# Optimization experiments

Hardware: AMD Instinct MI355X
Metric: run time of the kernel (lower is better)

## Reference

```python
import jax, jax.numpy as jnp
import numpy as np

NUM_HEADS = 4
HEAD_DIM = 64
IN_CH = 192
KERNEL_SIZES = (3, 5, 7, 9)  # per-head neighborhood size
NEG_INF = -1e30


def setup_inputs() -> dict:
    key = jax.random.key(0)
    k1, k2, k3 = jax.random.split(key, 3)
    x = jax.random.normal(k1, (8, IN_CH, 96, 96), dtype=jnp.float32)
    # QKV conv: out_channels = head_dim * num_heads * 3 = 768, 3x3, pad 1
    w_qkv = jax.random.normal(k2, (HEAD_DIM * NUM_HEADS * 3, IN_CH, 3, 3), dtype=jnp.float32) * 0.02
    b_qkv = jax.random.normal(k3, (HEAD_DIM * NUM_HEADS * 3,), dtype=jnp.float32) * 0.02
    return {"x": x, "w_qkv": w_qkv, "b_qkv": b_qkv}


def _neighborhood_attention(q, k, v, ksize):
    # q, k, v: [N, H, W, D]; KxK zero-padded neighborhood attention with
    # out-of-bounds positions masked out.
    N, H, W, D = q.shape
    pad = ksize // 2
    kp = jnp.pad(k, ((0, 0), (pad, pad), (pad, pad), (0, 0)))
    vp = jnp.pad(v, ((0, 0), (pad, pad), (pad, pad), (0, 0)))
    scale = 1.0 / np.sqrt(D).astype(np.float32)
    rows = jnp.arange(H)
    cols = jnp.arange(W)
    scores, masks = [], []
    for di in range(ksize):
        for dj in range(ksize):
            k_sh = kp[:, di:di + H, dj:dj + W, :]           # shifted keys
            scores.append(jnp.einsum('nhwd,nhwd->nhw', q, k_sh))
            rv = (rows + di - pad >= 0) & (rows + di - pad < H)   # [H]
            cv = (cols + dj - pad >= 0) & (cols + dj - pad < W)   # [W]
            masks.append(rv[:, None] & cv[None, :])               # [H, W]
    scores = jnp.stack(scores, axis=-1) * scale                   # [N,H,W,K2]
    mask = jnp.stack(masks, axis=-1)[None]                        # [1,H,W,K2]
    scores = jnp.where(mask, scores, NEG_INF)
    attn = jax.nn.softmax(scores, axis=-1)                        # [N,H,W,K2]
    out = jnp.zeros_like(q)
    t = 0
    for di in range(ksize):
        for dj in range(ksize):
            out = out + attn[..., t, None] * vp[:, di:di + H, dj:dj + W, :]
            t += 1
    return out  # [N,H,W,D]


def reference(x, w_qkv, b_qkv):
    # Dense QKV projection (Conv2d, stride 1, padding 1 == SAME for k=3)
    qkv = jax.lax.conv_general_dilated(
        x, w_qkv, window_strides=(1, 1), padding='SAME',
        dimension_numbers=('NCHW', 'OIHW', 'NCHW'))
    qkv = qkv + b_qkv[None, :, None, None]
    # transform_to_nhw1c: NCHW -> NHWC, then split channels into
    # num_heads blocks of 3*head_dim, each split into q, k, v.
    N, C, H, W = qkv.shape
    qkv = jnp.transpose(qkv, (0, 2, 3, 1)).reshape(N, H, W, NUM_HEADS, 3, HEAD_DIM)
    outs = []
    for h, ks in enumerate(KERNEL_SIZES):
        q = qkv[..., h, 0, :]
        k = qkv[..., h, 1, :]
        v = qkv[..., h, 2, :]
        o = _neighborhood_attention(q, k, v, ks)       # [N,H,W,D]
        outs.append(jnp.transpose(o, (0, 3, 1, 2)))    # transform_from_nhw1c -> NCHW
    return jnp.stack(outs, axis=0)  # [num_heads, N, D, H, W]
```

## Files before the change

kernel.cpp:

```cpp
#include <hip/hip_runtime.h>
#include <hip/hip_bf16.h>

#define NH 96
#define NW 96
#define NB 8
#define CIN 192
#define COUT 768
#define PH 98

typedef __attribute__((ext_vector_type(8))) unsigned short ushort8;
typedef __attribute__((ext_vector_type(8))) short bf16x8;
typedef __attribute__((ext_vector_type(4))) float f32x4;

static __device__ __forceinline__ unsigned short f2bf(float f) {
    unsigned int u = __float_as_uint(f);
    return (unsigned short)((u + 0x7fffu + ((u >> 16) & 1u)) >> 16);
}

typedef const __attribute__((address_space(1))) unsigned int gu32;
typedef __attribute__((address_space(3))) unsigned int lu32;
static __device__ __forceinline__ void gload16(const void* g, void* l) {
    __builtin_amdgcn_global_load_lds((gu32*)g, (lu32*)l, 16, 0, 0);
}

__global__ __launch_bounds__(256) void pack_x_kernel(
    const float* __restrict__ x, unsigned short* __restrict__ xp)
{
    __shared__ float tile[32][97];
    int bid = blockIdx.x;
    int ct = bid % 6; int y = (bid / 6) % NH; int n = bid / (6 * NH);
    int tid = threadIdx.x;
    int c0 = ct * 32;
    for (int i = tid; i < 32 * 96; i += 256) {
        int c = i / 96, xx = i % 96;
        tile[c][xx] = x[(((size_t)n * CIN + c0 + c) * NH + y) * NW + xx];
    }
    __syncthreads();
    for (int i = tid; i < 96 * 4; i += 256) {
        int xx = i >> 2, ch = i & 3;
        ushort8 pk;
#pragma unroll
        for (int j = 0; j < 8; ++j) pk[j] = f2bf(tile[ch * 8 + j][xx]);
        *(ushort8*)(xp + ((size_t)(n * PH + y + 1) * PH + xx + 1) * CIN + c0 + ch * 8) = pk;
    }
}

__global__ __launch_bounds__(256) void pack_w_kernel(
    const float* __restrict__ w, unsigned short* __restrict__ bw)
{
    __shared__ float ls[1728];
    int co = blockIdx.x; int tid = threadIdx.x;
    for (int i = tid; i < 1728; i += 256) ls[i] = w[(size_t)co * 1728 + i];
    __syncthreads();
    for (int i = tid; i < 1728; i += 256) {
        int sh = i / 192, ci = i % 192;
        bw[(size_t)co * 1728 + i] = f2bf(ls[ci * 9 + sh]);
    }
}

__global__ __launch_bounds__(512) void conv_gemm_kernel(
    const unsigned short* __restrict__ xp, const unsigned short* __restrict__ bw,
    const float* __restrict__ bias, unsigned short* __restrict__ qkq,
    unsigned short* __restrict__ vt)
{
    __shared__ __align__(16) char smem[131072];
    int bid = (blockIdx.x & 7) * 108 + (blockIdx.x >> 3);
    int brow = (bid / 3) * 256, bcol = (bid % 3) * 256;
    int tid = threadIdx.x, lane = tid & 63;
    int wid = tid >> 6, wm = wid >> 2, wn = wid & 3;
    int g = lane >> 4;

    const unsigned short* srcA[2][2];
    const unsigned short* srcB[2][2];
#pragma unroll
    for (int h = 0; h < 2; ++h)
#pragma unroll
        for (int i = 0; i < 2; ++i) {
            int s = i * 512 + tid;
            int rl = s >> 3, c = s & 7;
            int csw = (c ^ (rl & 7)) << 3;
            int p = brow + h * 128 + rl;
            int n = p / 9216; int rem = p - n * 9216;
            int y = rem / 96; int xx = rem - y * 96;
            srcA[h][i] = xp + ((size_t)(n * PH + y) * PH + xx) * CIN + csw;
            srcB[h][i] = bw + (size_t)(bcol + h * 128 + rl) * 1728 + csw;
        }
    int dsto[2];
#pragma unroll
    for (int i = 0; i < 2; ++i) dsto[i] = (i * 512 + (tid & ~63)) * 16;

#define STAGEU(T, U, BUF)                                                      \
    {                                                                          \
        int shift_ = (T) / 3, kk_ = (T) % 3;                                   \
        if ((U) < 2) {                                                         \
            int aO_ = ((shift_ / 3) * PH + (shift_ % 3)) * CIN + kk_ * 64;     \
            _Pragma("unroll")                                                  \
            for (int i_ = 0; i_ < 2; ++i_)                                     \
                gload16(srcA[(U)][i_] + aO_,                                   \
                        smem + (BUF) + (U) * 16384 + dsto[i_]);                \
        } else {                                                               \
            int bO_ = (T) * 64;                                                \
            _Pragma("unroll")                                                  \
            for (int i_ = 0; i_ < 2; ++i_)                                     \
                gload16(srcB[(U) - 2][i_] + bO_,                               \
                        smem + (BUF) + 32768 + ((U) - 2) * 16384 + dsto[i_]);  \
        }                                                                      \
    }

    int arow[8], brow_[4], xof[2];
#pragma unroll
    for (int m = 0; m < 8; ++m)
        arow[m] = (wm * 128 + m * 16 + (lane & 15)) * 128;
#pragma unroll
    for (int n = 0; n < 4; ++n)
        brow_[n] = 32768 + (wn * 64 + n * 16 + (lane & 15)) * 128;
#pragma unroll
    for (int kk = 0; kk < 2; ++kk)
        xof[kk] = ((kk * 4 + g) ^ (lane & 7)) << 4;

    STAGEU(0, 0, 0); STAGEU(0, 1, 0); STAGEU(0, 2, 0); STAGEU(0, 3, 0);

    f32x4 acc[8][4] = {};

    for (int t = 0; t < 27; ++t) {
        asm volatile("s_waitcnt vmcnt(0)" ::: "memory");
        __builtin_amdgcn_s_barrier();
        __builtin_amdgcn_sched_barrier(0);
        const int cur = (t & 1) << 16;
        const int nxt = cur ^ 65536;
        bf16x8 bf[4][2];
#pragma unroll
        for (int n = 0; n < 4; ++n)
#pragma unroll
            for (int kk = 0; kk < 2; ++kk)
                bf[n][kk] = *(const bf16x8*)(smem + cur + brow_[n] + xof[kk]);
#pragma unroll
        for (int p = 0; p < 4; ++p) {
            if (t < 26) STAGEU(t + 1, p, nxt);
            bf16x8 af[2][2];
#pragma unroll
            for (int mm = 0; mm < 2; ++mm)
#pragma unroll
                for (int kk = 0; kk < 2; ++kk)
                    af[mm][kk] = *(const bf16x8*)(smem + cur + arow[2 * p + mm] + xof[kk]);
            __builtin_amdgcn_s_setprio(1);
#pragma unroll
            for (int mm = 0; mm < 2; ++mm)
#pragma unroll
                for (int n = 0; n < 4; ++n)
#pragma unroll
                    for (int kk = 0; kk < 2; ++kk)
                        acc[2 * p + mm][n] = __builtin_amdgcn_mfma_f32_16x16x32_bf16(
                            af[mm][kk], bf[n][kk], acc[2 * p + mm][n], 0, 0, 0);
            __builtin_amdgcn_s_setprio(0);
        }
    }

    __syncthreads();
    unsigned short* sc = (unsigned short*)smem;
    float bn[4];
#pragma unroll
    for (int n = 0; n < 4; ++n)
        bn[n] = bias[bcol + wn * 64 + n * 16 + (lane & 15)];
#pragma unroll
    for (int m = 0; m < 8; ++m)
#pragma unroll
        for (int n = 0; n < 4; ++n) {
            int col = wn * 64 + n * 16 + (lane & 15);
            int cabs = bcol + col;
            float scale = ((cabs % 192) < 64) ? 0.125f : 1.0f;
#pragma unroll
            for (int j = 0; j < 4; ++j) {
                int row = wm * 128 + m * 16 + (lane >> 4) * 4 + j;
                sc[row * 256 + (col ^ ((row & 7) << 3))] =
                    f2bf((acc[m][n][j] + bn[n]) * scale);
            }
        }
    __syncthreads();
#pragma unroll
    for (int i = 0; i < 16; ++i) {
        int idx = i * 512 + tid;
        int row = idx >> 5, ch = idx & 31;
        int c0 = bcol + ch * 8;
        int r192 = c0 % 192;
        if (r192 < 128) {
            ushort8 pk = *(const ushort8*)(sc + row * 256 + ((ch * 8) ^ ((row & 7) << 3)));
            *(ushort8*)(qkq + (size_t)(brow + row) * 512 + (c0 / 192) * 128 + r192) = pk;
        }
    }
    int nblk = brow / 9216;
    int prem = brow - nblk * 9216;
#pragma unroll
    for (int h = 0; h < 4; ++h) {
        int lc = h * 192 + 128 - bcol;
        if (lc < 0 || lc > 192) continue;
        unsigned short* vth = vt + (size_t)h * 4718592;
#pragma unroll
        for (int it = 0; it < 4; ++it) {
            int i = it * 512 + tid;
            int d = i & 63, pxb = i >> 6;
            ushort8 pk;
#pragma unroll
            for (int j = 0; j < 8; ++j) {
                int px = pxb * 8 + j;
                pk[j] = sc[px * 256 + ((lc + d) ^ ((px & 7) << 3))];
            }
            *(ushort8*)(vth + ((size_t)(nblk * 64 + d)) * 9216 + prem + pxb * 8) = pk;
        }
    }
}

#define SLAB 24576
template<int KS>
static __device__ __forceinline__ void na_body(
    const unsigned short* __restrict__ qkq, const unsigned short* __restrict__ vt,
    float* __restrict__ out, int head, int bid, char* nsm)
{
    constexpr int PAD = KS / 2;
    int yp = bid % 48, n = bid / 48;
    int y0 = yp * 2;
    int tid = threadIdx.x;
    int wv = tid >> 6, lane = tid & 63;
    int g = lane >> 4, pix = lane & 15;
    int x0 = wv * 16;
    int x = x0 + pix;
    int W = x0 - 8;

    size_t qb0 = ((size_t)((n * 96 + y0) * 96 + x)) * 512 + (size_t)head * 128;
    size_t qb1 = qb0 + 96 * 512;
    bf16x8 qa0 = *(const bf16x8*)(qkq + qb0 + g * 8);
    bf16x8 qa1 = *(const bf16x8*)(qkq + qb0 + 32 + g * 8);
    bf16x8 qc0 = *(const bf16x8*)(qkq + qb1 + g * 8);
    bf16x8 qc1 = *(const bf16x8*)(qkq + qb1 + 32 + g * 8);
    asm volatile("s_waitcnt vmcnt(0)" ::: "memory");

    const size_t hoff = (size_t)head * 128 + 64;
#define STAGEKV(DI, BUF)                                                       \
    {                                                                          \
        int iy_ = min(max(y0 + (DI) - PAD, 0), 95);                            \
        size_t rb_ = ((size_t)((n * 96 + iy_) * 96)) * 512 + hoff;             \
        _Pragma("unroll")                                                      \
        for (int i_ = 0; i_ < 2; ++i_) {                                       \
            int ch_ = i_ * 384 + tid;                                          \
            int xx_ = ch_ >> 3, c8_ = (ch_ & 7) ^ (xx_ & 7);                   \
            gload16(qkq + rb_ + (size_t)xx_ * 512 + c8_ * 8,                   \
                    nsm + (BUF) * SLAB + (i_ * 384 + (tid & ~63)) * 16);       \
        }                                                                      \
        _Pragma("unroll")                                                      \
        for (int i_ = 0; i_ < 2; ++i_) {                                       \
            int ch_ = i_ * 384 + tid;                                          \
            int d_ = ch_ / 12, c_ = ch_ % 12;                                  \
            int cs_ = c_ ^ ((d_ >> 1) & 3);                                    \
            gload16(vt + (((size_t)(n * 64 + d_) * 96 + iy_)) * 96 + cs_ * 8,  \
                    nsm + (BUF) * SLAB + 12288 + (i_ * 384 + (tid & ~63)) * 16); \
        }                                                                      \
    }

    STAGEKV(0, 0);
    STAGEKV(1, 1);

    float l0 = 0.f, l1 = 0.f;
    f32x4 O0[4] = {}, O1[4] = {};
    int addrA = ((2 * (g & 1)) * 16 + pix) * 4;
    int addrB = addrA + 64;
    bool kthi = (g >> 1) != 0;
    int cxg = min(max(2 * wv - 1 + g, 0), 11);
    int vbase = 12288 + pix * 192 + ((cxg ^ ((pix >> 1) & 3)) << 4);

#define ROWCOMP(QF0, QF1, L, O)                                                \
    {                                                                          \
        unsigned int w0[2], w1[2];                                             \
        _Pragma("unroll")                                                      \
        for (int kt = 0; kt < 2; ++kt) {                                       \
            f32x4 tt = {};                                                     \
            tt = __builtin_amdgcn_mfma_f32_16x16x32_bf16(kf0[kt], QF0, tt, 0, 0, 0); \
            tt = __builtin_amdgcn_mfma_f32_16x16x32_bf16(kf1[kt], QF1, tt, 0, 0, 0); \
            float p[4];                                                        \
            _Pragma("unroll")                                                  \
            for (int r = 0; r < 4; ++r) {                                      \
                int kix = W + kt * 16 + g * 4 + r;                             \
                bool valid = ((unsigned)(kix - x + PAD) <= (unsigned)(2 * PAD)) && \
                             ((unsigned)kix < 96u);                            \
                p[r] = valid ? __expf(tt[r]) : 0.f;                            \
            }                                                                  \
            L += (p[0] + p[1]) + (p[2] + p[3]);                                \
            asm("v_cvt_pk_bf16_f32 %0, %1, %2" : "=v"(w0[kt]) : "v"(p[0]), "v"(p[1])); \
            asm("v_cvt_pk_bf16_f32 %0, %1, %2" : "=v"(w1[kt]) : "v"(p[2]), "v"(p[3])); \
        }                                                                      \
        int a0 = __builtin_amdgcn_ds_bpermute(addrA, (int)w0[0]);              \
        int b0 = __builtin_amdgcn_ds_bpermute(addrA, (int)w0[1]);              \
        int a1 = __builtin_amdgcn_ds_bpermute(addrA, (int)w1[0]);              \
        int b1 = __builtin_amdgcn_ds_bpermute(addrA, (int)w1[1]);              \
        int a2 = __builtin_amdgcn_ds_bpermute(addrB, (int)w0[0]);              \
        int b2 = __builtin_amdgcn_ds_bpermute(addrB, (int)w0[1]);              \
        int a3 = __builtin_amdgcn_ds_bpermute(addrB, (int)w1[0]);              \
        int b3 = __builtin_amdgcn_ds_bpermute(addrB, (int)w1[1]);              \
        union { int u[4]; bf16x8 v; } pa;                                      \
        pa.u[0] = kthi ? b0 : a0;                                              \
        pa.u[1] = kthi ? b1 : a1;                                              \
        pa.u[2] = kthi ? b2 : a2;                                              \
        pa.u[3] = kthi ? b3 : a3;                                              \
        _Pragma("unroll")                                                      \
        for (int dc = 0; dc < 4; ++dc)                                         \
            O[dc] = __builtin_amdgcn_mfma_f32_16x16x32_bf16(pa.v, vf[dc], O[dc], 0, 0, 0); \
    }

#pragma unroll
    for (int di = 0; di <= KS; ++di) {
        if (di < KS) asm volatile("s_waitcnt vmcnt(4)" ::: "memory");
        else         asm volatile("s_waitcnt vmcnt(0)" ::: "memory");
        __builtin_amdgcn_s_barrier();
        __builtin_amdgcn_sched_barrier(0);
        if (di + 2 <= KS) STAGEKV(di + 2, (di + 2) % 3);
        int iy = y0 + di - PAD;
        if (iy < 0 || iy >= 96) continue;
        const char* kb = nsm + (di % 3) * SLAB;

        bf16x8 kf0[2], kf1[2];
#pragma unroll
        for (int kt = 0; kt < 2; ++kt) {
            int kix_l = W + kt * 16 + pix;
            int ixc = min(max(kix_l, 0), 95);
            const char* kr = kb + ixc * 128;
            kf0[kt] = *(const bf16x8*)(kr + ((g ^ (ixc & 7)) << 4));
            kf1[kt] = *(const bf16x8*)(kr + (((4 + g) ^ (ixc & 7)) << 4));
        }
        bf16x8 vf[4];
#pragma unroll
        for (int dc = 0; dc < 4; ++dc)
            vf[dc] = *(const bf16x8*)(kb + dc * 3072 + vbase);

        if (di < KS)  ROWCOMP(qa0, qa1, l0, O0);
        if (di >= 1)  ROWCOMP(qc0, qc1, l1, O1);
    }

    l0 += __shfl_xor(l0, 16, 64); l0 += __shfl_xor(l0, 32, 64);
    l1 += __shfl_xor(l1, 16, 64); l1 += __shfl_xor(l1, 32, 64);
    float li0 = 1.0f / l0, li1 = 1.0f / l1;
    float lj0[4], lj1[4];
#pragma unroll
    for (int j = 0; j < 4; ++j) {
        lj0[j] = __uint_as_float((unsigned)__builtin_amdgcn_ds_bpermute(
            (4 * g + j) * 4, (int)__float_as_uint(li0)));
        lj1[j] = __uint_as_float((unsigned)__builtin_amdgcn_ds_bpermute(
            (4 * g + j) * 4, (int)__float_as_uint(li1)));
    }
    __syncthreads();
    float (*sO2)[64][97] = (float(*)[64][97])nsm;
#pragma unroll
    for (int dc = 0; dc < 4; ++dc)
#pragma unroll
        for (int j = 0; j < 4; ++j) {
            sO2[0][dc * 16 + pix][x0 + g * 4 + j] = O0[dc][j] * lj0[j];
            sO2[1][dc * 16 + pix][x0 + g * 4 + j] = O1[dc][j] * lj1[j];
        }
    __syncthreads();
    for (int i = tid; i < 3072; i += 384) {
        int r = i / 1536;
        int rem = i - r * 1536;
        int d = rem / 24, xq = rem % 24;
        float4 v4 = { sO2[r][d][xq * 4], sO2[r][d][xq * 4 + 1],
                      sO2[r][d][xq * 4 + 2], sO2[r][d][xq * 4 + 3] };
        *(float4*)(out + ((size_t)(head * 8 + n) * 64 + d) * 9216
                   + (y0 + r) * 96 + xq * 4) = v4;
    }
}

__global__ __launch_bounds__(384, 2) void na_mfma_all(
    const unsigned short* __restrict__ qkq, const unsigned short* __restrict__ vt,
    float* __restrict__ out)
{
    __shared__ __align__(16) char nsm[3 * SLAB];
    int head = blockIdx.x & 3;
    int bid = blockIdx.x >> 2;
    switch (head) {
        case 0: na_body<3>(qkq, vt,               out, 0, bid, nsm); break;
        case 1: na_body<5>(qkq, vt + 4718592,     out, 1, bid, nsm); break;
        case 2: na_body<7>(qkq, vt + 2 * 4718592, out, 2, bid, nsm); break;
        default: na_body<9>(qkq, vt + 3 * 4718592, out, 3, bid, nsm); break;
    }
}

extern "C" void kernel_launch(void* const* d_in, const int* in_sizes, int n_in,
                              void* d_out, int out_size, void* d_ws, size_t ws_size,
                              hipStream_t stream) {
    const float* x  = (const float*)d_in[0];
    const float* w  = (const float*)d_in[1];
    const float* b  = (const float*)d_in[2];
    float* out = (float*)d_out;

    unsigned short* qkq  = (unsigned short*)d_ws;
    unsigned short* vt   = (unsigned short*)((char*)d_ws + 75497472);
    unsigned short* xpad = (unsigned short*)((char*)d_ws + 113246208);
    unsigned short* bw   = (unsigned short*)((char*)d_ws + 142749696);

    hipMemsetAsync(xpad, 0, 29503488, stream);
    pack_x_kernel<<<NB * NH * 6, 256, 0, stream>>>(x, xpad);
    pack_w_kernel<<<COUT, 256, 0, stream>>>(w, bw);
    conv_gemm_kernel<<<864, 512, 0, stream>>>(xpad, bw, b, qkq, vt);

    na_mfma_all<<<4 * 384, 384, 0, stream>>>(qkq, vt, out);
}
```

Baseline: 321.7 us.

## Prepack weights in MFMA fragment order and load B directly to registers

Weights are now packed into the exact per-lane MFMA fragment layout, so the conv GEMM reads B fragments straight from global memory into registers, double-buffered across k-tiles, instead of staging them through LDS. This halves the LDS footprint (128KB to 64KB), which may allow two blocks per CU, and removes B-side LDS reads. The epilogue is split into two half-tile passes to fit the smaller shared buffer. The cost is more global-load latency exposed on the B path, more registers held for two fragment sets, and extra barriers in the epilogue.

```diff
diff --git a/kernel.cpp b/kernel.cpp
--- a/kernel.cpp
+++ b/kernel.cpp
@@ -45,33 +45,81 @@
     }
 }
 
-__global__ __launch_bounds__(256) void pack_w_kernel(
-    const float* __restrict__ w, unsigned short* __restrict__ bw)
+__global__ __launch_bounds__(256) void pack_wf_kernel(
+    const float* __restrict__ w, unsigned short* __restrict__ bwf)
 {
-    __shared__ float ls[1728];
-    int co = blockIdx.x; int tid = threadIdx.x;
-    for (int i = tid; i < 1728; i += 256) ls[i] = w[(size_t)co * 1728 + i];
-    __syncthreads();
-    for (int i = tid; i < 1728; i += 256) {
-        int sh = i / 192, ci = i % 192;
-        bw[(size_t)co * 1728 + i] = f2bf(ls[ci * 9 + sh]);
-    }
-}
+    int j = blockIdx.x * 256 + threadIdx.x;
+    int lane = j & 63;
+    int fg = j >> 6;
+    int kk = fg & 1, n = (fg >> 1) & 3, wn = (fg >> 3) & 3;
+    int kt = (fg >> 5) % 27, ct = fg / 864;
+    int co = ct * 256 + wn * 64 + n * 16 + (lane & 15);
+    int kb = kt * 64 + kk * 32 + (lane >> 4) * 8;
+    ushort8 pk;
+#pragma unroll
+    for (int e = 0; e < 8; ++e) {
+        int k = kb + e;
+        int sh = k / 192, ci = k - sh * 192;
+        pk[e] = f2bf(w[(size_t)co * 1728 + ci * 9 + sh]);
+    }
+    *(ushort8*)(bwf + (size_t)j * 8) = pk;
+}
+
+#define CONVTILE(T, BFCUR, BFNXT, LAST)                                        \
+    {                                                                          \
+        asm volatile("s_waitcnt vmcnt(0)" ::: "memory");                       \
+        __builtin_amdgcn_s_barrier();                                          \
+        __builtin_amdgcn_sched_barrier(0);                                     \
+        const int cur_ = ((T) & 1) << 15;                                      \
+        const int nxt_ = cur_ ^ 32768;                                         \
+        _Pragma("unroll")                                                      \
+        for (int p_ = 0; p_ < 4; ++p_) {                                       \
+            if (!(LAST)) {                                                     \
+                int shift_ = ((T) + 1) / 3, kk_ = ((T) + 1) % 3;               \
+                int aO_ = ((shift_ / 3) * PH + (shift_ % 3)) * CIN + kk_ * 64; \
+                gload16(srcA[p_ >> 1][p_ & 1] + aO_,                           \
+                        smem + nxt_ + dsto[p_ >> 1][p_ & 1]);                  \
+                BFNXT[p_][0] = *(const bf16x8*)(pB + ((T) + 1) * 16384 +       \
+                                                (p_ * 2 + 0) * 512);           \
+                BFNXT[p_][1] = *(const bf16x8*)(pB + ((T) + 1) * 16384 +       \
+                                                (p_ * 2 + 1) * 512);           \
+            }                                                                  \
+            bf16x8 af_[2][2];                                                  \
+            _Pragma("unroll")                                                  \
+            for (int mm_ = 0; mm_ < 2; ++mm_)                                  \
+                _Pragma("unroll")                                              \
+                for (int k2_ = 0; k2_ < 2; ++k2_)                              \
+                    af_[mm_][k2_] = *(const bf16x8*)(smem + cur_ +             \
+                        arow[2 * p_ + mm_] + xof[k2_]);                        \
+            __builtin_amdgcn_s_setprio(1);                                     \
+            _Pragma("unroll")                                                  \
+            for (int mm_ = 0; mm_ < 2; ++mm_)                                  \
+                _Pragma("unroll")                                              \
+                for (int n_ = 0; n_ < 4; ++n_)                                 \
+                    _Pragma("unroll")                                          \
+                    for (int k2_ = 0; k2_ < 2; ++k2_)                          \
+                        acc[2 * p_ + mm_][n_] =                                \
+                            __builtin_amdgcn_mfma_f32_16x16x32_bf16(           \
+                                af_[mm_][k2_], BFCUR[n_][k2_],                 \
+                                acc[2 * p_ + mm_][n_], 0, 0, 0);               \
+            __builtin_amdgcn_s_setprio(0);                                     \
+        }                                                                      \
+    }
 
 __global__ __launch_bounds__(512) void conv_gemm_kernel(
-    const unsigned short* __restrict__ xp, const unsigned short* __restrict__ bw,
+    const unsigned short* __restrict__ xp, const unsigned short* __restrict__ bwf,
     const float* __restrict__ bias, unsigned short* __restrict__ qkq,
     unsigned short* __restrict__ vt)
 {
-    __shared__ __align__(16) char smem[131072];
+    __shared__ __align__(16) char smem[65536];
     int bid = (blockIdx.x & 7) * 108 + (blockIdx.x >> 3);
-    int brow = (bid / 3) * 256, bcol = (bid % 3) * 256;
+    int brow = (bid / 3) * 256, bcol = (bid % 3) * 256, ct = bid % 3;
     int tid = threadIdx.x, lane = tid & 63;
     int wid = tid >> 6, wm = wid >> 2, wn = wid & 3;
     int g = lane >> 4;
 
     const unsigned short* srcA[2][2];
-    const unsigned short* srcB[2][2];
+    int dsto[2][2];
 #pragma unroll
     for (int h = 0; h < 2; ++h)
 #pragma unroll
@@ -83,78 +131,38 @@
             int n = p / 9216; int rem = p - n * 9216;
             int y = rem / 96; int xx = rem - y * 96;
             srcA[h][i] = xp + ((size_t)(n * PH + y) * PH + xx) * CIN + csw;
-            srcB[h][i] = bw + (size_t)(bcol + h * 128 + rl) * 1728 + csw;
-        }
-    int dsto[2];
-#pragma unroll
-    for (int i = 0; i < 2; ++i) dsto[i] = (i * 512 + (tid & ~63)) * 16;
-
-#define STAGEU(T, U, BUF)                                                      \
-    {                                                                          \
-        int shift_ = (T) / 3, kk_ = (T) % 3;                                   \
-        if ((U) < 2) {                                                         \
-            int aO_ = ((shift_ / 3) * PH + (shift_ % 3)) * CIN + kk_ * 64;     \
-            _Pragma("unroll")                                                  \
-            for (int i_ = 0; i_ < 2; ++i_)                                     \
-                gload16(srcA[(U)][i_] + aO_,                                   \
-                        smem + (BUF) + (U) * 16384 + dsto[i_]);                \
-        } else {                                                               \
-            int bO_ = (T) * 64;                                                \
-            _Pragma("unroll")                                                  \
-            for (int i_ = 0; i_ < 2; ++i_)                                     \
-                gload16(srcB[(U) - 2][i_] + bO_,                               \
-                        smem + (BUF) + 32768 + ((U) - 2) * 16384 + dsto[i_]);  \
-        }                                                                      \
-    }
-
-    int arow[8], brow_[4], xof[2];
+            dsto[h][i] = h * 16384 + (i * 512 + (tid & ~63)) * 16;
+        }
+
+    const unsigned short* pB = bwf + (size_t)ct * 27 * 16384 + wn * 4096 + lane * 8;
+
+    int arow[8], xof[2];
 #pragma unroll
     for (int m = 0; m < 8; ++m)
         arow[m] = (wm * 128 + m * 16 + (lane & 15)) * 128;
 #pragma unroll
-    for (int n = 0; n < 4; ++n)
-        brow_[n] = 32768 + (wn * 64 + n * 16 + (lane & 15)) * 128;
-#pragma unroll
     for (int kk = 0; kk < 2; ++kk)
         xof[kk] = ((kk * 4 + g) ^ (lane & 7)) << 4;
 
-    STAGEU(0, 0, 0); STAGEU(0, 1, 0); STAGEU(0, 2, 0); STAGEU(0, 3, 0);
+#pragma unroll
+    for (int h = 0; h < 2; ++h)
+#pragma unroll
+        for (int i = 0; i < 2; ++i)
+            gload16(srcA[h][i], smem + dsto[h][i]);
+    bf16x8 bfA[4][2], bfB[4][2];
+#pragma unroll
+    for (int n = 0; n < 4; ++n)
+#pragma unroll
+        for (int kk = 0; kk < 2; ++kk)
+            bfA[n][kk] = *(const bf16x8*)(pB + (n * 2 + kk) * 512);
 
     f32x4 acc[8][4] = {};
 
-    for (int t = 0; t < 27; ++t) {
-        asm volatile("s_waitcnt vmcnt(0)" ::: "memory");
-        __builtin_amdgcn_s_barrier();
-        __builtin_amdgcn_sched_barrier(0);
-        const int cur = (t & 1) << 16;
-        const int nxt = cur ^ 65536;
-        bf16x8 bf[4][2];
-#pragma unroll
-        for (int n = 0; n < 4; ++n)
-#pragma unroll
-            for (int kk = 0; kk < 2; ++kk)
-                bf[n][kk] = *(const bf16x8*)(smem + cur + brow_[n] + xof[kk]);
-#pragma unroll
-        for (int p = 0; p < 4; ++p) {
-            if (t < 26) STAGEU(t + 1, p, nxt);
-            bf16x8 af[2][2];
-#pragma unroll
-            for (int mm = 0; mm < 2; ++mm)
-#pragma unroll
-                for (int kk = 0; kk < 2; ++kk)
-                    af[mm][kk] = *(const bf16x8*)(smem + cur + arow[2 * p + mm] + xof[kk]);
-            __builtin_amdgcn_s_setprio(1);
-#pragma unroll
-            for (int mm = 0; mm < 2; ++mm)
-#pragma unroll
-                for (int n = 0; n < 4; ++n)
-#pragma unroll
-                    for (int kk = 0; kk < 2; ++kk)
-                        acc[2 * p + mm][n] = __builtin_amdgcn_mfma_f32_16x16x32_bf16(
-                            af[mm][kk], bf[n][kk], acc[2 * p + mm][n], 0, 0, 0);
-            __builtin_amdgcn_s_setprio(0);
-        }
-    }
+    for (int u = 0; u < 13; ++u) {
+        CONVTILE(2 * u,     bfA, bfB, 0);
+        CONVTILE(2 * u + 1, bfB, bfA, 0);
+    }
+    CONVTILE(26, bfA, bfB, 1);
 
     __syncthreads();
     unsigned short* sc = (unsigned short*)smem;
@@ -162,51 +170,59 @@
 #pragma unroll
     for (int n = 0; n < 4; ++n)
         bn[n] = bias[bcol + wn * 64 + n * 16 + (lane & 15)];
-#pragma unroll
-    for (int m = 0; m < 8; ++m)
-#pragma unroll
-        for (int n = 0; n < 4; ++n) {
-            int col = wn * 64 + n * 16 + (lane & 15);
-            int cabs = bcol + col;
-            float scale = ((cabs % 192) < 64) ? 0.125f : 1.0f;
-#pragma unroll
-            for (int j = 0; j < 4; ++j) {
-                int row = wm * 128 + m * 16 + (lane >> 4) * 4 + j;
-                sc[row * 256 + (col ^ ((row & 7) << 3))] =
-                    f2bf((acc[m][n][j] + bn[n]) * scale);
-            }
-        }
-    __syncthreads();
-#pragma unroll
-    for (int i = 0; i < 16; ++i) {
-        int idx = i * 512 + tid;
-        int row = idx >> 5, ch = idx & 31;
-        int c0 = bcol + ch * 8;
-        int r192 = c0 % 192;
-        if (r192 < 128) {
-            ushort8 pk = *(const ushort8*)(sc + row * 256 + ((ch * 8) ^ ((row & 7) << 3)));
-            *(ushort8*)(qkq + (size_t)(brow + row) * 512 + (c0 / 192) * 128 + r192) = pk;
-        }
-    }
     int nblk = brow / 9216;
     int prem = brow - nblk * 9216;
 #pragma unroll
-    for (int h = 0; h < 4; ++h) {
-        int lc = h * 192 + 128 - bcol;
-        if (lc < 0 || lc > 192) continue;
-        unsigned short* vth = vt + (size_t)h * 4718592;
-#pragma unroll
-        for (int it = 0; it < 4; ++it) {
-            int i = it * 512 + tid;
-            int d = i & 63, pxb = i >> 6;
-            ushort8 pk;
-#pragma unroll
-            for (int j = 0; j < 8; ++j) {
-                int px = pxb * 8 + j;
-                pk[j] = sc[px * 256 + ((lc + d) ^ ((px & 7) << 3))];
+    for (int p2 = 0; p2 < 2; ++p2) {
+        if (wm == p2) {
+#pragma unroll
+            for (int m = 0; m < 8; ++m)
+#pragma unroll
+                for (int n = 0; n < 4; ++n) {
+                    int col = wn * 64 + n * 16 + (lane & 15);
+                    int cabs = bcol + col;
+                    float scale = ((cabs % 192) < 64) ? 0.125f : 1.0f;
+#pragma unroll
+                    for (int j = 0; j < 4; ++j) {
+                        int row = m * 16 + (lane >> 4) * 4 + j;
+                        sc[row * 256 + (col ^ ((row & 7) << 3))] =
+                            f2bf((acc[m][n][j] + bn[n]) * scale);
+                    }
+                }
+        }
+        __syncthreads();
+#pragma unroll
+        for (int i = 0; i < 8; ++i) {
+            int idx = i * 512 + tid;
+            int row = idx >> 5, ch = idx & 31;
+            int c0 = bcol + ch * 8;
+            int r192 = c0 % 192;
+            if (r192 < 128) {
+                ushort8 pk = *(const ushort8*)(sc + row * 256 + ((ch * 8) ^ ((row & 7) << 3)));
+                *(ushort8*)(qkq + (size_t)(brow + p2 * 128 + row) * 512
+                            + (c0 / 192) * 128 + r192) = pk;
             }
-            *(ushort8*)(vth + ((size_t)(nblk * 64 + d)) * 9216 + prem + pxb * 8) = pk;
-        }
+        }
+#pragma unroll
+        for (int h = 0; h < 4; ++h) {
+            int lc = h * 192 + 128 - bcol;
+            if (lc < 0 || lc > 192) continue;
+            unsigned short* vth = vt + (size_t)h * 4718592;
+#pragma unroll
+            for (int it = 0; it < 2; ++it) {
+                int i = it * 512 + tid;
+                int d = i & 63, pxb = i >> 6;
+                ushort8 pk;
+#pragma unroll
+                for (int j = 0; j < 8; ++j) {
+                    int px = pxb * 8 + j;
+                    pk[j] = sc[px * 256 + ((lc + d) ^ ((px & 7) << 3))];
+                }
+                *(ushort8*)(vth + ((size_t)(nblk * 64 + d)) * 9216
+                            + prem + p2 * 128 + pxb * 8) = pk;
+            }
+        }
+        __syncthreads();
     }
 }
 
@@ -392,12 +408,12 @@
     unsigned short* qkq  = (unsigned short*)d_ws;
     unsigned short* vt   = (unsigned short*)((char*)d_ws + 75497472);
     unsigned short* xpad = (unsigned short*)((char*)d_ws + 113246208);
-    unsigned short* bw   = (unsigned short*)((char*)d_ws + 142749696);
+    unsigned short* bwf  = (unsigned short*)((char*)d_ws + 142749696);
 
     hipMemsetAsync(xpad, 0, 29503488, stream);
     pack_x_kernel<<<NB * NH * 6, 256, 0, stream>>>(x, xpad);
-    pack_w_kernel<<<COUT, 256, 0, stream>>>(w, bw);
-    conv_gemm_kernel<<<864, 512, 0, stream>>>(xpad, bw, b, qkq, vt);
+    pack_wf_kernel<<<648, 256, 0, stream>>>(w, bwf);
+    conv_gemm_kernel<<<864, 512, 0, stream>>>(xpad, bwf, b, qkq, vt);
 
     na_mfma_all<<<4 * 384, 384, 0, stream>>>(qkq, vt, out);
 }
```

Result: slower. 328.7 us (+2.2%).

## Process three output rows per neighborhood-attention block to reuse staged K/V rows

Applied to the files above, without the earlier changes.

Each attention block now computes three output rows instead of two, so every staged K/V row in shared memory serves up to three query rows. This cuts redundant K/V loads by reducing the number of row-halo reloads, and drops the grid from 1536 to 1024 blocks. It adds a third accumulator set, which raises register pressure, and enlarges the shared-memory output staging buffer, which may reduce occupancy below the two blocks per CU requested in launch bounds.

```diff
diff --git a/kernel.cpp b/kernel.cpp
--- a/kernel.cpp
+++ b/kernel.cpp
@@ -217,8 +217,8 @@
     float* __restrict__ out, int head, int bid, char* nsm)
 {
     constexpr int PAD = KS / 2;
-    int yp = bid % 48, n = bid / 48;
-    int y0 = yp * 2;
+    int yp = bid % 32, n = bid / 32;
+    int y0 = yp * 3;
     int tid = threadIdx.x;
     int wv = tid >> 6, lane = tid & 63;
     int g = lane >> 4, pix = lane & 15;
@@ -227,11 +227,12 @@
     int W = x0 - 8;
 
     size_t qb0 = ((size_t)((n * 96 + y0) * 96 + x)) * 512 + (size_t)head * 128;
-    size_t qb1 = qb0 + 96 * 512;
     bf16x8 qa0 = *(const bf16x8*)(qkq + qb0 + g * 8);
     bf16x8 qa1 = *(const bf16x8*)(qkq + qb0 + 32 + g * 8);
-    bf16x8 qc0 = *(const bf16x8*)(qkq + qb1 + g * 8);
-    bf16x8 qc1 = *(const bf16x8*)(qkq + qb1 + 32 + g * 8);
+    bf16x8 qc0 = *(const bf16x8*)(qkq + qb0 + 96 * 512 + g * 8);
+    bf16x8 qc1 = *(const bf16x8*)(qkq + qb0 + 96 * 512 + 32 + g * 8);
+    bf16x8 qe0 = *(const bf16x8*)(qkq + qb0 + 2 * 96 * 512 + g * 8);
+    bf16x8 qe1 = *(const bf16x8*)(qkq + qb0 + 2 * 96 * 512 + 32 + g * 8);
     asm volatile("s_waitcnt vmcnt(0)" ::: "memory");
 
     const size_t hoff = (size_t)head * 128 + 64;
@@ -259,8 +260,8 @@
     STAGEKV(0, 0);
     STAGEKV(1, 1);
 
-    float l0 = 0.f, l1 = 0.f;
-    f32x4 O0[4] = {}, O1[4] = {};
+    float l0 = 0.f, l1 = 0.f, l2 = 0.f;
+    f32x4 O0[4] = {}, O1[4] = {}, O2[4] = {};
     int addrA = ((2 * (g & 1)) * 16 + pix) * 4;
     int addrB = addrA + 64;
     bool kthi = (g >> 1) != 0;
@@ -306,12 +307,12 @@
     }
 
 #pragma unroll
-    for (int di = 0; di <= KS; ++di) {
-        if (di < KS) asm volatile("s_waitcnt vmcnt(4)" ::: "memory");
-        else         asm volatile("s_waitcnt vmcnt(0)" ::: "memory");
+    for (int di = 0; di <= KS + 1; ++di) {
+        if (di <= KS) asm volatile("s_waitcnt vmcnt(4)" ::: "memory");
+        else          asm volatile("s_waitcnt vmcnt(0)" ::: "memory");
         __builtin_amdgcn_s_barrier();
         __builtin_amdgcn_sched_barrier(0);
-        if (di + 2 <= KS) STAGEKV(di + 2, (di + 2) % 3);
+        if (di + 2 <= KS + 1) STAGEKV(di + 2, (di + 2) % 3);
         int iy = y0 + di - PAD;
         if (iy < 0 || iy >= 96) continue;
         const char* kb = nsm + (di % 3) * SLAB;
@@ -330,37 +331,42 @@
         for (int dc = 0; dc < 4; ++dc)
             vf[dc] = *(const bf16x8*)(kb + dc * 3072 + vbase);
 
-        if (di < KS)  ROWCOMP(qa0, qa1, l0, O0);
-        if (di >= 1)  ROWCOMP(qc0, qc1, l1, O1);
+        if (di < KS)              ROWCOMP(qa0, qa1, l0, O0);
+        if (di >= 1 && di <= KS)  ROWCOMP(qc0, qc1, l1, O1);
+        if (di >= 2)              ROWCOMP(qe0, qe1, l2, O2);
     }
 
     l0 += __shfl_xor(l0, 16, 64); l0 += __shfl_xor(l0, 32, 64);
     l1 += __shfl_xor(l1, 16, 64); l1 += __shfl_xor(l1, 32, 64);
-    float li0 = 1.0f / l0, li1 = 1.0f / l1;
-    float lj0[4], lj1[4];
+    l2 += __shfl_xor(l2, 16, 64); l2 += __shfl_xor(l2, 32, 64);
+    float li0 = 1.0f / l0, li1 = 1.0f / l1, li2 = 1.0f / l2;
+    float lj0[4], lj1[4], lj2[4];
 #pragma unroll
     for (int j = 0; j < 4; ++j) {
         lj0[j] = __uint_as_float((unsigned)__builtin_amdgcn_ds_bpermute(
             (4 * g + j) * 4, (int)__float_as_uint(li0)));
         lj1[j] = __uint_as_float((unsigned)__builtin_amdgcn_ds_bpermute(
             (4 * g + j) * 4, (int)__float_as_uint(li1)));
-    }
-    __syncthreads();
-    float (*sO2)[64][97] = (float(*)[64][97])nsm;
+        lj2[j] = __uint_as_float((unsigned)__builtin_amdgcn_ds_bpermute(
+            (4 * g + j) * 4, (int)__float_as_uint(li2)));
+    }
+    __syncthreads();
+    float (*sO3)[64][97] = (float(*)[64][97])nsm;
 #pragma unroll
     for (int dc = 0; dc < 4; ++dc)
 #pragma unroll
         for (int j = 0; j < 4; ++j) {
-            sO2[0][dc * 16 + pix][x0 + g * 4 + j] = O0[dc][j] * lj0[j];
-            sO2[1][dc * 16 + pix][x0 + g * 4 + j] = O1[dc][j] * lj1[j];
-        }
-    __syncthreads();
-    for (int i = tid; i < 3072; i += 384) {
+            sO3[0][dc * 16 + pix][x0 + g * 4 + j] = O0[dc][j] * lj0[j];
+            sO3[1][dc * 16 + pix][x0 + g * 4 + j] = O1[dc][j] * lj1[j];
+            sO3[2][dc * 16 + pix][x0 + g * 4 + j] = O2[dc][j] * lj2[j];
+        }
+    __syncthreads();
+    for (int i = tid; i < 4608; i += 384) {
         int r = i / 1536;
         int rem = i - r * 1536;
         int d = rem / 24, xq = rem % 24;
-        float4 v4 = { sO2[r][d][xq * 4], sO2[r][d][xq * 4 + 1],
-                      sO2[r][d][xq * 4 + 2], sO2[r][d][xq * 4 + 3] };
+        float4 v4 = { sO3[r][d][xq * 4], sO3[r][d][xq * 4 + 1],
+                      sO3[r][d][xq * 4 + 2], sO3[r][d][xq * 4 + 3] };
         *(float4*)(out + ((size_t)(head * 8 + n) * 64 + d) * 9216
                    + (y0 + r) * 96 + xq * 4) = v4;
     }
@@ -370,7 +376,7 @@
     const unsigned short* __restrict__ qkq, const unsigned short* __restrict__ vt,
     float* __restrict__ out)
 {
-    __shared__ __align__(16) char nsm[3 * SLAB];
+    __shared__ __align__(16) char nsm[74496];
     int head = blockIdx.x & 3;
     int bid = blockIdx.x >> 2;
     switch (head) {
@@ -399,5 +405,5 @@
     pack_w_kernel<<<COUT, 256, 0, stream>>>(w, bw);
     conv_gemm_kernel<<<864, 512, 0, stream>>>(xpad, bw, b, qkq, vt);
 
-    na_mfma_all<<<4 * 384, 384, 0, stream>>>(qkq, vt, out);
-}
+    na_mfma_all<<<4 * 256, 384, 0, stream>>>(qkq, vt, out);
+}
```

After: 317.4 us. About the same (-1.4%).
